# Performance work log

Measured on AMD Instinct MI355X. Metric: run time of the kernel, lower is better.

Reference implementation:

```python
import jax, jax.numpy as jnp
import numpy as np

T = 4096      # number of parser actions / steps
V = 100000    # word vocab
NPOS = 48
WE, PE, AE = 300, 32, 64
H = 512       # hidden_size == input_size
NA = 100      # num_actions = len(productions) + 2


def setup_inputs() -> dict:
    key = jax.random.key(0)
    ks = jax.random.split(key, 24)
    def n(i, shape, s=0.05):
        return jax.random.normal(ks[i], shape, dtype=jnp.float32) * s
    def enc(i):
        # (wih, whh, bih, bhh, h0, c0) for one StackLSTM (num_layers=1)
        k1, k2 = jax.random.split(ks[i])
        return (jax.random.normal(k1, (4 * H, H), jnp.float32) * 0.05,
                jax.random.normal(k2, (4 * H, H), jnp.float32) * 0.05,
                jnp.zeros((4 * H,), jnp.float32), jnp.zeros((4 * H,), jnp.float32),
                jnp.zeros((H,), jnp.float32), jnp.zeros((H,), jnp.float32))
    s = enc(10); b = enc(11); h = enc(12)
    return {
        'words': jax.random.randint(ks[0], (T,), 0, V),
        'pos_tags': jax.random.randint(ks[1], (T,), 0, NPOS),
        'actions': jax.random.randint(ks[2], (T,), 0, NA),
        'word_emb': n(3, (V, WE), 0.1),
        'pos_emb': n(4, (NPOS, PE), 0.1),
        'act_emb': n(5, (NA, AE), 0.1),
        'w2e_w': n(6, (H, WE + PE)), 'w2e_b': jnp.zeros((H,), jnp.float32),
        'a2e_w': n(7, (H, AE)), 'a2e_b': jnp.zeros((H,), jnp.float32),
        'stk_wih': s[0], 'stk_whh': s[1], 'stk_bih': s[2], 'stk_bhh': s[3], 'stk_h0': s[4], 'stk_c0': s[5],
        'buf_wih': b[0], 'buf_whh': b[1], 'buf_bih': b[2], 'buf_bhh': b[3], 'buf_h0': b[4], 'buf_c0': b[5],
        'hist_wih': h[0], 'hist_whh': h[1], 'hist_bih': h[2], 'hist_bhh': h[3], 'hist_h0': h[4], 'hist_c0': h[5],
        'sum_w': n(8, (H, 3 * H)), 'sum_b': jnp.zeros((H,), jnp.float32),
        'out_w': n(9, (NA, H)), 'out_b': jnp.zeros((NA,), jnp.float32),
    }


def _lstm_cell(x, hc, wih, whh, bih, bhh):
    # single-timestep LSTM step, PyTorch gate order (i, f, g, o)
    h, c = hc
    g = x @ wih.T + h @ whh.T + (bih + bhh)
    i, f, gg, o = jnp.split(g, 4, axis=-1)
    c2 = jax.nn.sigmoid(f) * c + jax.nn.sigmoid(i) * jnp.tanh(gg)
    h2 = jax.nn.sigmoid(o) * jnp.tanh(c2)
    return (h2, c2)


def _forward(words, pos_tags, actions,
             word_emb, pos_emb, act_emb, w2e_w, w2e_b, a2e_w, a2e_b,
             stk_wih, stk_whh, stk_bih, stk_bhh, stk_h0, stk_c0,
             buf_wih, buf_whh, buf_bih, buf_bhh, buf_h0, buf_c0,
             hist_wih, hist_whh, hist_bih, hist_bhh, hist_h0, hist_c0,
             sum_w, sum_b, out_w, out_b):
    # vectorized embedding lookups + word2encoder / action2encoder projections
    xw = jax.nn.relu(jnp.concatenate([word_emb[words], pos_emb[pos_tags]], -1) @ w2e_w.T + w2e_b)  # [T,H]
    xa = jax.nn.relu(act_emb[actions] @ a2e_w.T + a2e_b)                                           # [T,H]

    def step(carry, xs):
        hs, hb, hh = carry
        x_w, x_a = xs
        # action log-probs computed from current encoder tops (before this step's pushes)
        top = jnp.concatenate([hs[0], hb[0], hh[0]])            # [3H]
        summary = jnp.tanh(top @ sum_w.T + sum_b)               # encoders2summary (dropout=0)
        logp = jax.nn.log_softmax(summary @ out_w.T + out_b)    # [NA]
        hs = _lstm_cell(x_w, hs, stk_wih, stk_whh, stk_bih, stk_bhh)
        hb = _lstm_cell(x_w, hb, buf_wih, buf_whh, buf_bih, buf_bhh)
        hh = _lstm_cell(x_a, hh, hist_wih, hist_whh, hist_bih, hist_bhh)
        return (hs, hb, hh), logp

    init = ((stk_h0, stk_c0), (buf_h0, buf_c0), (hist_h0, hist_c0))
    _, logps = jax.lax.scan(step, init, (xw, xa))
    return logps  # [T, NA]


def reference(words, pos_tags, actions,
              word_emb, pos_emb, act_emb, w2e_w, w2e_b, a2e_w, a2e_b,
              stk_wih, stk_whh, stk_bih, stk_bhh, stk_h0, stk_c0,
              buf_wih, buf_whh, buf_bih, buf_bhh, buf_h0, buf_c0,
              hist_wih, hist_whh, hist_bih, hist_bhh, hist_h0, hist_c0,
              sum_w, sum_b, out_w, out_b):
    return _forward(words, pos_tags, actions,
                    word_emb, pos_emb, act_emb, w2e_w, w2e_b, a2e_w, a2e_b,
                    stk_wih, stk_whh, stk_bih, stk_bhh, stk_h0, stk_c0,
                    buf_wih, buf_whh, buf_bih, buf_bhh, buf_h0, buf_c0,
                    hist_wih, hist_whh, hist_bih, hist_bhh, hist_h0, hist_c0,
                    sum_w, sum_b, out_w, out_b)
```

## Files before the change

kernel.cpp:

```cpp
#include <hip/hip_runtime.h>
#include <stdint.h>

#define TT 4096
#define HH 512
#define GG 2048
#define NS 64

typedef unsigned long long u64;

__device__ __forceinline__ float sigm(float x) { return 1.0f / (1.0f + __expf(-x)); }
__device__ __forceinline__ float tanh_fast(float x) {
    x = fminf(20.0f, fmaxf(-20.0f, x));
    float e = __expf(2.0f * x);
    return (e - 1.0f) / (e + 1.0f);
}

__global__ __launch_bounds__(256) void k_xw(
    const int* __restrict__ words, const int* __restrict__ pos,
    const float* __restrict__ wemb, const float* __restrict__ pemb,
    const float* __restrict__ W, const float* __restrict__ b,
    float* __restrict__ out)
{
    __shared__ float xr[8][336];
    const int t0 = blockIdx.x * 8, tid = threadIdx.x;
    for (int s = 0; s < 8; ++s) {
        int w = words[t0 + s], p = pos[t0 + s];
        for (int i = tid; i < 332; i += 256)
            xr[s][i] = (i < 300) ? wemb[(size_t)w * 300 + i] : pemb[p * 32 + (i - 300)];
    }
    __syncthreads();
    const int o1 = tid, o2 = tid + 256;
    float acc[8][2] = {};
    for (int k = 0; k < 332; ++k) {
        float wa = W[(size_t)o1 * 332 + k];
        float wb = W[(size_t)o2 * 332 + k];
#pragma unroll
        for (int s = 0; s < 8; ++s) {
            float x = xr[s][k];
            acc[s][0] += wa * x;
            acc[s][1] += wb * x;
        }
    }
#pragma unroll
    for (int s = 0; s < 8; ++s) {
        out[(size_t)(t0 + s) * 512 + o1] = fmaxf(acc[s][0] + b[o1], 0.0f);
        out[(size_t)(t0 + s) * 512 + o2] = fmaxf(acc[s][1] + b[o2], 0.0f);
    }
}

__global__ __launch_bounds__(256) void k_xa(
    const int* __restrict__ acts, const float* __restrict__ aemb,
    const float* __restrict__ W, const float* __restrict__ b,
    float* __restrict__ out)
{
    __shared__ float xr[8][68];
    const int t0 = blockIdx.x * 8, tid = threadIdx.x;
    for (int s = 0; s < 8; ++s) {
        int a = acts[t0 + s];
        if (tid < 64) xr[s][tid] = aemb[(size_t)a * 64 + tid];
    }
    __syncthreads();
    const int o1 = tid, o2 = tid + 256;
    float acc[8][2] = {};
    for (int k = 0; k < 64; ++k) {
        float wa = W[(size_t)o1 * 64 + k];
        float wb = W[(size_t)o2 * 64 + k];
#pragma unroll
        for (int s = 0; s < 8; ++s) {
            float x = xr[s][k];
            acc[s][0] += wa * x;
            acc[s][1] += wb * x;
        }
    }
#pragma unroll
    for (int s = 0; s < 8; ++s) {
        out[(size_t)(t0 + s) * 512 + o1] = fmaxf(acc[s][0] + b[o1], 0.0f);
        out[(size_t)(t0 + s) * 512 + o2] = fmaxf(acc[s][1] + b[o2], 0.0f);
    }
}

__global__ __launch_bounds__(256) void gemm_nt(
    const float* __restrict__ A, const float* __restrict__ B, float* __restrict__ C,
    const float* __restrict__ b1, const float* __restrict__ b2,
    int M, int N, int K, int op)
{
    __shared__ __align__(16) float As[16][68];
    __shared__ __align__(16) float Bs[16][68];
    const int tid = threadIdx.x;
    const int bm = blockIdx.y * 64, bn = blockIdx.x * 64;
    const int lr = tid >> 2, lc = tid & 3;
    const int tm = tid & 15, tn = tid >> 4;
    float acc[4][4] = {};
    for (int k0 = 0; k0 < K; k0 += 16) {
        float4 a4 = *(const float4*)(A + (size_t)(bm + lr) * K + k0 + lc * 4);
        float4 b4 = *(const float4*)(B + (size_t)(bn + lr) * K + k0 + lc * 4);
        As[lc * 4 + 0][lr] = a4.x; As[lc * 4 + 1][lr] = a4.y;
        As[lc * 4 + 2][lr] = a4.z; As[lc * 4 + 3][lr] = a4.w;
        Bs[lc * 4 + 0][lr] = b4.x; Bs[lc * 4 + 1][lr] = b4.y;
        Bs[lc * 4 + 2][lr] = b4.z; Bs[lc * 4 + 3][lr] = b4.w;
        __syncthreads();
#pragma unroll
        for (int k = 0; k < 16; ++k) {
            const float4 av = *(const float4*)&As[k][tm * 4];
            const float4 bv = *(const float4*)&Bs[k][tn * 4];
            acc[0][0] += av.x * bv.x; acc[0][1] += av.x * bv.y; acc[0][2] += av.x * bv.z; acc[0][3] += av.x * bv.w;
            acc[1][0] += av.y * bv.x; acc[1][1] += av.y * bv.y; acc[1][2] += av.y * bv.z; acc[1][3] += av.y * bv.w;
            acc[2][0] += av.z * bv.x; acc[2][1] += av.z * bv.y; acc[2][2] += av.z * bv.z; acc[2][3] += av.z * bv.w;
            acc[3][0] += av.w * bv.x; acc[3][1] += av.w * bv.y; acc[3][2] += av.w * bv.z; acc[3][3] += av.w * bv.w;
        }
        __syncthreads();
    }
#pragma unroll
    for (int i = 0; i < 4; ++i) {
        const int r = bm + tm * 4 + i;
#pragma unroll
        for (int j = 0; j < 4; ++j) {
            const int cc = bn + tn * 4 + j;
            float v = acc[i][j] + b1[cc];
            if (b2) v += b2[cc];
            if (op == 1) v = tanh_fast(v);
            C[(size_t)r * N + cc] = v;
        }
    }
}

#define LDW(i) const float4 w##i = wp[i];
#define DOT(i) { float4 hv = hq[i]; \
    acc = fmaf(w##i.x, hv.x, acc); acc = fmaf(w##i.y, hv.y, acc); \
    acc = fmaf(w##i.z, hv.z, acc); acc = fmaf(w##i.w, hv.w, acc); }

__global__ __launch_bounds__(256, 1) void scan_kernel(
    const float* __restrict__ gx,
    const float* __restrict__ whh0, const float* __restrict__ whh1, const float* __restrict__ whh2,
    const float* __restrict__ h00, const float* __restrict__ h01, const float* __restrict__ h02,
    const float* __restrict__ c00, const float* __restrict__ c01, const float* __restrict__ c02,
    u64* __restrict__ hbuf,
    float* __restrict__ htop)
{
    const int chain = blockIdx.x / NS;
    const int slice = blockIdx.x % NS;
    const int tid = threadIdx.x;
    const int r = tid >> 3;
    const int k = tid & 7;
    const int gate = r >> 3;
    const int j = r & 7;
    const int grow = gate * HH + slice * 8 + j;

    const float* whh = (chain == 0) ? whh0 : (chain == 1) ? whh1 : whh2;
    const float* h0  = (chain == 0) ? h00  : (chain == 1) ? h01  : h02;
    const float* c0  = (chain == 0) ? c00  : (chain == 1) ? c01  : c02;
    const float* gxc = gx + (size_t)chain * TT * GG;

    const float4* wp = (const float4*)(whh + (size_t)grow * HH + k * 64);
    LDW(0) LDW(1) LDW(2) LDW(3) LDW(4) LDW(5) LDW(6) LDW(7)
    LDW(8) LDW(9) LDW(10) LDW(11) LDW(12) LDW(13) LDW(14) LDW(15)

    float c_reg = 0.0f;
    if (tid < 8) {
        c_reg = c0[slice * 8 + tid];
        float hv = h0[slice * 8 + tid];
        u64 pv = ((u64)1u << 32) | (u64)__float_as_uint(hv);
        __hip_atomic_store(&hbuf[(size_t)chain * HH + slice * 8 + tid], pv,
                           __ATOMIC_RELAXED, __HIP_MEMORY_SCOPE_AGENT);
        htop[(size_t)chain * HH + slice * 8 + tid] = hv;
    }

    __shared__ float h_lds[8 * 68];
    __shared__ float gsum[32];

    for (int t = 0; t < TT; ++t) {
        float gxv = 0.0f;
        if (k == 0) gxv = gxc[(size_t)t * GG + grow];

        if (tid < 64) {
            const u64* src = hbuf + (size_t)((t & 1) * 3 + chain) * HH + tid * 8;
            const unsigned need = (unsigned)(t + 1);
            u64 p0, p1, p2, p3, p4, p5, p6, p7;
            for (;;) {
                p0 = __hip_atomic_load(src + 0, __ATOMIC_RELAXED, __HIP_MEMORY_SCOPE_AGENT);
                p1 = __hip_atomic_load(src + 1, __ATOMIC_RELAXED, __HIP_MEMORY_SCOPE_AGENT);
                p2 = __hip_atomic_load(src + 2, __ATOMIC_RELAXED, __HIP_MEMORY_SCOPE_AGENT);
                p3 = __hip_atomic_load(src + 3, __ATOMIC_RELAXED, __HIP_MEMORY_SCOPE_AGENT);
                p4 = __hip_atomic_load(src + 4, __ATOMIC_RELAXED, __HIP_MEMORY_SCOPE_AGENT);
                p5 = __hip_atomic_load(src + 5, __ATOMIC_RELAXED, __HIP_MEMORY_SCOPE_AGENT);
                p6 = __hip_atomic_load(src + 6, __ATOMIC_RELAXED, __HIP_MEMORY_SCOPE_AGENT);
                p7 = __hip_atomic_load(src + 7, __ATOMIC_RELAXED, __HIP_MEMORY_SCOPE_AGENT);
                int ok = (unsigned)(p0 >> 32) >= need && (unsigned)(p1 >> 32) >= need &&
                         (unsigned)(p2 >> 32) >= need && (unsigned)(p3 >> 32) >= need &&
                         (unsigned)(p4 >> 32) >= need && (unsigned)(p5 >> 32) >= need &&
                         (unsigned)(p6 >> 32) >= need && (unsigned)(p7 >> 32) >= need;
                if (__all(ok)) break;
                __builtin_amdgcn_s_sleep(1);
            }
            float4* d = (float4*)(h_lds + (tid >> 3) * 68 + (tid & 7) * 8);
            d[0] = make_float4(__uint_as_float((unsigned)p0), __uint_as_float((unsigned)p1),
                               __uint_as_float((unsigned)p2), __uint_as_float((unsigned)p3));
            d[1] = make_float4(__uint_as_float((unsigned)p4), __uint_as_float((unsigned)p5),
                               __uint_as_float((unsigned)p6), __uint_as_float((unsigned)p7));
        }
        __syncthreads();

        const float4* hq = (const float4*)(h_lds + k * 68);
        float acc = 0.0f;
        DOT(0) DOT(1) DOT(2) DOT(3) DOT(4) DOT(5) DOT(6) DOT(7)
        DOT(8) DOT(9) DOT(10) DOT(11) DOT(12) DOT(13) DOT(14) DOT(15)
        acc += __shfl_xor(acc, 1);
        acc += __shfl_xor(acc, 2);
        acc += __shfl_xor(acc, 4);
        if (k == 0) gsum[r] = acc + gxv;
        __syncthreads();

        if (tid < 8) {
            float gi = gsum[tid], gf = gsum[8 + tid], gg = gsum[16 + tid], go = gsum[24 + tid];
            float c2 = sigm(gf) * c_reg + sigm(gi) * tanh_fast(gg);
            float h2 = sigm(go) * tanh_fast(c2);
            c_reg = c2;
            u64 pv = ((u64)(unsigned)(t + 2) << 32) | (u64)__float_as_uint(h2);
            __hip_atomic_store(&hbuf[(size_t)(((t + 1) & 1) * 3 + chain) * HH + slice * 8 + tid],
                               pv, __ATOMIC_RELAXED, __HIP_MEMORY_SCOPE_AGENT);
            if (t + 1 < TT)
                htop[(size_t)(t + 1) * 1536 + chain * HH + slice * 8 + tid] = h2;
        }
        __syncthreads();
    }
}

__global__ __launch_bounds__(128) void k_logp(
    const float* __restrict__ summ, const float* __restrict__ Wo,
    const float* __restrict__ bo, float* __restrict__ out)
{
    __shared__ float srow[512];
    __shared__ float z[104];
    __shared__ float red[2];
    const int t = blockIdx.x, tid = threadIdx.x;
    ((float4*)srow)[tid] = ((const float4*)(summ + (size_t)t * 512))[tid];
    __syncthreads();
    if (tid < 100) {
        float a = bo[tid];
        const float* wr = Wo + (size_t)tid * 512;
        for (int k = 0; k < 512; k += 4)
            a += wr[k] * srow[k] + wr[k + 1] * srow[k + 1] + wr[k + 2] * srow[k + 2] + wr[k + 3] * srow[k + 3];
        z[tid] = a;
    }
    __syncthreads();
    if (tid < 64) {
        float m = z[tid];
        if (tid + 64 < 100) m = fmaxf(m, z[tid + 64]);
#pragma unroll
        for (int off = 32; off >= 1; off >>= 1) m = fmaxf(m, __shfl_xor(m, off, 64));
        float e = __expf(z[tid] - m) + ((tid + 64 < 100) ? __expf(z[tid + 64] - m) : 0.0f);
#pragma unroll
        for (int off = 32; off >= 1; off >>= 1) e += __shfl_xor(e, off, 64);
        if (tid == 0) { red[0] = m; red[1] = __logf(e); }
    }
    __syncthreads();
    if (tid < 100) out[(size_t)t * 100 + tid] = z[tid] - red[0] - red[1];
}

extern "C" void kernel_launch(void* const* d_in, const int* in_sizes, int n_in,
                              void* d_out, int out_size, void* d_ws, size_t ws_size,
                              hipStream_t stream)
{
    const int* words = (const int*)d_in[0];
    const int* pos   = (const int*)d_in[1];
    const int* acts  = (const int*)d_in[2];
    const float* wemb  = (const float*)d_in[3];
    const float* pemb  = (const float*)d_in[4];
    const float* aemb  = (const float*)d_in[5];
    const float* w2e_w = (const float*)d_in[6];
    const float* w2e_b = (const float*)d_in[7];
    const float* a2e_w = (const float*)d_in[8];
    const float* a2e_b = (const float*)d_in[9];
    const float* sum_w = (const float*)d_in[28];
    const float* sum_b = (const float*)d_in[29];
    const float* out_w = (const float*)d_in[30];
    const float* out_b = (const float*)d_in[31];

    float* ws = (float*)d_ws;
    float* xw   = ws;
    float* xa   = xw + (size_t)TT * HH;
    float* gxp  = xa + (size_t)TT * HH;
    float* htop = gxp + (size_t)3 * TT * GG;
    u64*   hbuf = (u64*)(htop + (size_t)TT * 3 * HH);
    float* summary = xw;

    hipMemsetAsync(hbuf, 0, 2 * 3 * HH * sizeof(u64), stream);

    k_xw<<<dim3(TT / 8), dim3(256), 0, stream>>>(words, pos, wemb, pemb, w2e_w, w2e_b, xw);
    k_xa<<<dim3(TT / 8), dim3(256), 0, stream>>>(acts, aemb, a2e_w, a2e_b, xa);

    dim3 g2(GG / 64, TT / 64);
    gemm_nt<<<g2, dim3(256), 0, stream>>>(xw, (const float*)d_in[10], gxp,
                                          (const float*)d_in[12], (const float*)d_in[13],
                                          TT, GG, HH, 0);
    gemm_nt<<<g2, dim3(256), 0, stream>>>(xw, (const float*)d_in[16], gxp + (size_t)TT * GG,
                                          (const float*)d_in[18], (const float*)d_in[19],
                                          TT, GG, HH, 0);
    gemm_nt<<<g2, dim3(256), 0, stream>>>(xa, (const float*)d_in[22], gxp + (size_t)2 * TT * GG,
                                          (const float*)d_in[24], (const float*)d_in[25],
                                          TT, GG, HH, 0);

    scan_kernel<<<dim3(3 * NS), dim3(256), 0, stream>>>(
        gxp,
        (const float*)d_in[11], (const float*)d_in[17], (const float*)d_in[23],
        (const float*)d_in[14], (const float*)d_in[20], (const float*)d_in[26],
        (const float*)d_in[15], (const float*)d_in[21], (const float*)d_in[27],
        hbuf, htop);

    dim3 g3(HH / 64, TT / 64);
    gemm_nt<<<g3, dim3(256), 0, stream>>>(htop, sum_w, summary, sum_b, nullptr,
                                          TT, HH, 3 * HH, 1);
    k_logp<<<dim3(TT), dim3(128), 0, stream>>>(summary, out_w, out_b, (float*)d_out);
}
```

Before: 9.330 ms.

## Restructure LSTM scan into fewer 1024-thread blocks with shuffle-based gate combine

```diff
diff --git a/kernel.cpp b/kernel.cpp
--- a/kernel.cpp
+++ b/kernel.cpp
@@ -4,7 +4,7 @@
 #define TT 4096
 #define HH 512
 #define GG 2048
-#define NS 64
+#define NS 16
 
 typedef unsigned long long u64;
 
@@ -124,12 +124,14 @@
     }
 }
 
-#define LDW(i) const float4 w##i = wp[i];
+#define LDW(i) float4 q##i = wp[i];
+#define SPL(i) float a##i##x = q##i.x, a##i##y = q##i.y, a##i##z = q##i.z, a##i##w = q##i.w;
+#define PIN(i) asm volatile("" : "+v"(a##i##x), "+v"(a##i##y), "+v"(a##i##z), "+v"(a##i##w));
 #define DOT(i) { float4 hv = hq[i]; \
-    acc = fmaf(w##i.x, hv.x, acc); acc = fmaf(w##i.y, hv.y, acc); \
-    acc = fmaf(w##i.z, hv.z, acc); acc = fmaf(w##i.w, hv.w, acc); }
-
-__global__ __launch_bounds__(256, 1) void scan_kernel(
+    acc = fmaf(a##i##x, hv.x, acc); acc = fmaf(a##i##y, hv.y, acc); \
+    acc = fmaf(a##i##z, hv.z, acc); acc = fmaf(a##i##w, hv.w, acc); }
+
+__global__ __launch_bounds__(1024, 4) void scan_kernel(
     const float* __restrict__ gx,
     const float* __restrict__ whh0, const float* __restrict__ whh1, const float* __restrict__ whh2,
     const float* __restrict__ h00, const float* __restrict__ h01, const float* __restrict__ h02,
@@ -140,88 +142,77 @@
     const int chain = blockIdx.x / NS;
     const int slice = blockIdx.x % NS;
     const int tid = threadIdx.x;
-    const int r = tid >> 3;
-    const int k = tid & 7;
-    const int gate = r >> 3;
-    const int j = r & 7;
-    const int grow = gate * HH + slice * 8 + j;
+    const int out_j = tid >> 5;
+    const int gate  = (tid >> 3) & 3;
+    const int k     = tid & 7;
+    const int row   = gate * HH + slice * 32 + out_j;
+    const int lane  = tid & 63;
+    const int lbase = lane & 32;
 
     const float* whh = (chain == 0) ? whh0 : (chain == 1) ? whh1 : whh2;
     const float* h0  = (chain == 0) ? h00  : (chain == 1) ? h01  : h02;
     const float* c0  = (chain == 0) ? c00  : (chain == 1) ? c01  : c02;
     const float* gxc = gx + (size_t)chain * TT * GG;
 
-    const float4* wp = (const float4*)(whh + (size_t)grow * HH + k * 64);
+    const float4* wp = (const float4*)(whh + (size_t)row * HH + k * 64);
     LDW(0) LDW(1) LDW(2) LDW(3) LDW(4) LDW(5) LDW(6) LDW(7)
     LDW(8) LDW(9) LDW(10) LDW(11) LDW(12) LDW(13) LDW(14) LDW(15)
+    SPL(0) SPL(1) SPL(2) SPL(3) SPL(4) SPL(5) SPL(6) SPL(7)
+    SPL(8) SPL(9) SPL(10) SPL(11) SPL(12) SPL(13) SPL(14) SPL(15)
 
     float c_reg = 0.0f;
-    if (tid < 8) {
-        c_reg = c0[slice * 8 + tid];
-        float hv = h0[slice * 8 + tid];
+    if ((tid & 31) == 0) {
+        c_reg = c0[slice * 32 + out_j];
+        float hv = h0[slice * 32 + out_j];
         u64 pv = ((u64)1u << 32) | (u64)__float_as_uint(hv);
-        __hip_atomic_store(&hbuf[(size_t)chain * HH + slice * 8 + tid], pv,
+        __hip_atomic_store(&hbuf[(size_t)chain * HH + slice * 32 + out_j], pv,
                            __ATOMIC_RELAXED, __HIP_MEMORY_SCOPE_AGENT);
-        htop[(size_t)chain * HH + slice * 8 + tid] = hv;
-    }
-
-    __shared__ float h_lds[8 * 68];
-    __shared__ float gsum[32];
+        htop[(size_t)chain * HH + slice * 32 + out_j] = hv;
+    }
+
+    __shared__ float h_lds[2][8 * 68];
 
     for (int t = 0; t < TT; ++t) {
+        PIN(0) PIN(1) PIN(2) PIN(3) PIN(4) PIN(5) PIN(6) PIN(7)
+        PIN(8) PIN(9) PIN(10) PIN(11) PIN(12) PIN(13) PIN(14) PIN(15)
+        const int par = t & 1;
+
         float gxv = 0.0f;
-        if (k == 0) gxv = gxc[(size_t)t * GG + grow];
-
-        if (tid < 64) {
-            const u64* src = hbuf + (size_t)((t & 1) * 3 + chain) * HH + tid * 8;
+        if (k == 0) gxv = gxc[(size_t)t * GG + row];
+
+        if (tid < 512) {
+            const u64* src = hbuf + (size_t)(par * 3 + chain) * HH + tid;
             const unsigned need = (unsigned)(t + 1);
-            u64 p0, p1, p2, p3, p4, p5, p6, p7;
+            u64 p;
             for (;;) {
-                p0 = __hip_atomic_load(src + 0, __ATOMIC_RELAXED, __HIP_MEMORY_SCOPE_AGENT);
-                p1 = __hip_atomic_load(src + 1, __ATOMIC_RELAXED, __HIP_MEMORY_SCOPE_AGENT);
-                p2 = __hip_atomic_load(src + 2, __ATOMIC_RELAXED, __HIP_MEMORY_SCOPE_AGENT);
-                p3 = __hip_atomic_load(src + 3, __ATOMIC_RELAXED, __HIP_MEMORY_SCOPE_AGENT);
-                p4 = __hip_atomic_load(src + 4, __ATOMIC_RELAXED, __HIP_MEMORY_SCOPE_AGENT);
-                p5 = __hip_atomic_load(src + 5, __ATOMIC_RELAXED, __HIP_MEMORY_SCOPE_AGENT);
-                p6 = __hip_atomic_load(src + 6, __ATOMIC_RELAXED, __HIP_MEMORY_SCOPE_AGENT);
-                p7 = __hip_atomic_load(src + 7, __ATOMIC_RELAXED, __HIP_MEMORY_SCOPE_AGENT);
-                int ok = (unsigned)(p0 >> 32) >= need && (unsigned)(p1 >> 32) >= need &&
-                         (unsigned)(p2 >> 32) >= need && (unsigned)(p3 >> 32) >= need &&
-                         (unsigned)(p4 >> 32) >= need && (unsigned)(p5 >> 32) >= need &&
-                         (unsigned)(p6 >> 32) >= need && (unsigned)(p7 >> 32) >= need;
-                if (__all(ok)) break;
-                __builtin_amdgcn_s_sleep(1);
+                p = __hip_atomic_load(src, __ATOMIC_RELAXED, __HIP_MEMORY_SCOPE_AGENT);
+                if (__all((unsigned)(p >> 32) >= need)) break;
             }
-            float4* d = (float4*)(h_lds + (tid >> 3) * 68 + (tid & 7) * 8);
-            d[0] = make_float4(__uint_as_float((unsigned)p0), __uint_as_float((unsigned)p1),
-                               __uint_as_float((unsigned)p2), __uint_as_float((unsigned)p3));
-            d[1] = make_float4(__uint_as_float((unsigned)p4), __uint_as_float((unsigned)p5),
-                               __uint_as_float((unsigned)p6), __uint_as_float((unsigned)p7));
+            h_lds[par][(tid >> 6) * 68 + (tid & 63)] = __uint_as_float((unsigned)p);
         }
         __syncthreads();
 
-        const float4* hq = (const float4*)(h_lds + k * 68);
+        const float4* hq = (const float4*)(&h_lds[par][k * 68]);
         float acc = 0.0f;
         DOT(0) DOT(1) DOT(2) DOT(3) DOT(4) DOT(5) DOT(6) DOT(7)
         DOT(8) DOT(9) DOT(10) DOT(11) DOT(12) DOT(13) DOT(14) DOT(15)
         acc += __shfl_xor(acc, 1);
         acc += __shfl_xor(acc, 2);
         acc += __shfl_xor(acc, 4);
-        if (k == 0) gsum[r] = acc + gxv;
-        __syncthreads();
-
-        if (tid < 8) {
-            float gi = gsum[tid], gf = gsum[8 + tid], gg = gsum[16 + tid], go = gsum[24 + tid];
-            float c2 = sigm(gf) * c_reg + sigm(gi) * tanh_fast(gg);
+        if (k == 0) acc += gxv;
+        float gf = __shfl(acc, lbase + 8);
+        float gg = __shfl(acc, lbase + 16);
+        float go = __shfl(acc, lbase + 24);
+        if ((tid & 31) == 0) {
+            float c2 = sigm(gf) * c_reg + sigm(acc) * tanh_fast(gg);
             float h2 = sigm(go) * tanh_fast(c2);
             c_reg = c2;
             u64 pv = ((u64)(unsigned)(t + 2) << 32) | (u64)__float_as_uint(h2);
-            __hip_atomic_store(&hbuf[(size_t)(((t + 1) & 1) * 3 + chain) * HH + slice * 8 + tid],
+            __hip_atomic_store(&hbuf[(size_t)(((t + 1) & 1) * 3 + chain) * HH + slice * 32 + out_j],
                                pv, __ATOMIC_RELAXED, __HIP_MEMORY_SCOPE_AGENT);
             if (t + 1 < TT)
-                htop[(size_t)(t + 1) * 1536 + chain * HH + slice * 8 + tid] = h2;
-        }
-        __syncthreads();
+                htop[(size_t)(t + 1) * 1536 + chain * HH + slice * 32 + out_j] = h2;
+        }
     }
 }
 
@@ -284,7 +275,7 @@
     u64*   hbuf = (u64*)(htop + (size_t)TT * 3 * HH);
     float* summary = xw;
 
-    hipMemsetAsync(hbuf, 0, 2 * 3 * HH * sizeof(u64), stream);
+    (void)hipMemsetAsync(hbuf, 0, 2 * 3 * HH * sizeof(u64), stream);
 
     k_xw<<<dim3(TT / 8), dim3(256), 0, stream>>>(words, pos, wemb, pemb, w2e_w, w2e_b, xw);
     k_xa<<<dim3(TT / 8), dim3(256), 0, stream>>>(acts, aemb, a2e_w, a2e_b, xa);
@@ -300,7 +291,7 @@
                                           (const float*)d_in[24], (const float*)d_in[25],
                                           TT, GG, HH, 0);
 
-    scan_kernel<<<dim3(3 * NS), dim3(256), 0, stream>>>(
+    scan_kernel<<<dim3(3 * NS), dim3(1024), 0, stream>>>(
         gxp,
         (const float*)d_in[11], (const float*)d_in[17], (const float*)d_in[23],
         (const float*)d_in[14], (const float*)d_in[20], (const float*)d_in[26],
```

Result: slower. 10.89 ms (+16.7%).
